# Kernel tuning notes

Measured on AMD Instinct MI355X. Metric: run time of the kernel, lower is better.

The kernel has to match this reference:

```python
import jax, jax.numpy as jnp
import numpy as np

B, N, NODE_DIM, COND_DIM, EDGE_DIM = 16, 256, 512, 512, 128
E_TOT = 262144  # total edges, divisible by B
EPS = 1e-5


def weight_norm(v, g):
    # torch weight_norm dim=0: per-output-row normalization. v: [out, in], g: [out]
    return v * (g / jnp.sqrt(jnp.sum(v * v, axis=1)))[:, None]


def setup_inputs() -> dict:
    key = jax.random.key(0)
    ks = jax.random.split(key, 12)
    node_feats = jax.random.normal(ks[0], (B, N, NODE_DIM), dtype=jnp.float32)
    cond_feats = jax.random.normal(ks[1], (B, COND_DIM), dtype=jnp.float32)
    edge_indexes = jnp.sort(jax.random.randint(ks[2], (E_TOT,), 0, B * N * N, dtype=jnp.int64))
    s_node = 1.0 / np.sqrt(NODE_DIM)
    s_cond = 1.0 / np.sqrt(COND_DIM)
    s_film = 1.0 / np.sqrt(2 * EDGE_DIM)
    return {
        "node_feats": node_feats,
        "cond_feats": cond_feats,
        "edge_indexes": edge_indexes,
        "v_node": jax.random.uniform(ks[3], (EDGE_DIM, NODE_DIM), jnp.float32, -s_node, s_node),
        "g_node": jnp.ones((EDGE_DIM,), jnp.float32),
        "b_node": jnp.zeros((EDGE_DIM,), jnp.float32),
        "v_cond": jax.random.uniform(ks[4], (2 * EDGE_DIM, COND_DIM), jnp.float32, -s_cond, s_cond),
        "g_cond": jnp.ones((2 * EDGE_DIM,), jnp.float32),
        "b_cond": jnp.zeros((2 * EDGE_DIM,), jnp.float32),
        "w_film": jax.random.uniform(ks[5], (EDGE_DIM, 2 * EDGE_DIM), jnp.float32, -s_film, s_film),
        "b_film": jnp.zeros((EDGE_DIM,), jnp.float32),
    }


def reference(node_feats, cond_feats, edge_indexes, v_node, g_node, b_node,
              v_cond, g_cond, b_cond, w_film, b_film):
    # node projection: Dropout(0) -> weight_norm Linear -> ReLU
    w_n = weight_norm(v_node, g_node)
    nodes = jax.nn.relu(jnp.einsum('bnd,ed->bne', node_feats, w_n) + b_node)  # [B,N,E]

    # cond projection -> gamma, beta
    w_c = weight_norm(v_cond, g_cond)
    gb = cond_feats @ w_c.T + b_cond  # [B, 2E]
    gamma = gb[:, :EDGE_DIM] + 1.0
    beta = gb[:, EDGE_DIM:]

    # gather edge endpoints directly (equivalent to materializing [B,N,N,2E] 'cat' then indexing)
    b_idx = edge_indexes // (N * N)
    i_idx = (edge_indexes // N) % N
    j_idx = edge_indexes % N
    fused = jnp.concatenate([nodes[b_idx, i_idx], nodes[b_idx, j_idx]], axis=-1)  # [E_TOT, 2E]

    # film_l: linear -> LayerNorm(no affine) -> FiLM -> ReLU, on view (B, E_TOT//B, E)
    x = fused @ w_film.T + b_film  # [E_TOT, EDGE_DIM]
    x = x.reshape(B, E_TOT // B, EDGE_DIM)
    mu = jnp.mean(x, axis=-1, keepdims=True)
    var = jnp.mean(jnp.square(x - mu), axis=-1, keepdims=True)
    x = (x - mu) * jax.lax.rsqrt(var + EPS)
    x = x * gamma[:, None, :] + beta[:, None, :]
    x = jax.nn.relu(x)
    return x.reshape(E_TOT, EDGE_DIM)
```

## Files before the change

### kernel.cpp

```cpp
#include <hip/hip_runtime.h>
#include <hip/hip_bf16.h>

typedef __bf16 bf16_t;
typedef bf16_t bf16x8 __attribute__((ext_vector_type(8)));
typedef float f32x4 __attribute__((ext_vector_type(4)));

#define NODE_DIM 512
#define COND_DIM 512
#define EDGE_DIM 128

__global__ __launch_bounds__(256) void cond_scales_kernel(
    const float* __restrict__ cond_feats, const float* __restrict__ v_cond,
    const float* __restrict__ g_cond, const float* __restrict__ b_cond,
    const float* __restrict__ v_node, const float* __restrict__ g_node,
    float* __restrict__ gamma, float* __restrict__ beta,
    float* __restrict__ scale_node)
{
    int lane = threadIdx.x & 63;
    int wv = threadIdx.x >> 6;
    int bid = blockIdx.x;
    if (bid < 1024) {
        int id = bid * 4 + wv;
        int b = id >> 8, n = id & 255;
        const float* cf = cond_feats + b * COND_DIM + lane * 8;
        const float* vc = v_cond + (size_t)n * COND_DIM + lane * 8;
        float dot = 0.f, sq = 0.f;
#pragma unroll
        for (int i = 0; i < 2; i++) {
            float4 c4 = ((const float4*)cf)[i];
            float4 v4 = ((const float4*)vc)[i];
            dot += c4.x * v4.x + c4.y * v4.y + c4.z * v4.z + c4.w * v4.w;
            sq  += v4.x * v4.x + v4.y * v4.y + v4.z * v4.z + v4.w * v4.w;
        }
#pragma unroll
        for (int o = 32; o > 0; o >>= 1) {
            dot += __shfl_xor(dot, o);
            sq  += __shfl_xor(sq, o);
        }
        if (lane == 0) {
            float val = dot * (g_cond[n] * rsqrtf(sq)) + b_cond[n];
            if (n < 128) gamma[b * 128 + n] = val + 1.0f;
            else         beta[b * 128 + (n - 128)] = val;
        }
    } else {
        int id = (bid - 1024) * 4 + wv;
        const float* vn = v_node + (size_t)id * NODE_DIM + lane * 8;
        float sq = 0.f;
#pragma unroll
        for (int i = 0; i < 2; i++) {
            float4 v4 = ((const float4*)vn)[i];
            sq += v4.x * v4.x + v4.y * v4.y + v4.z * v4.z + v4.w * v4.w;
        }
#pragma unroll
        for (int o = 32; o > 0; o >>= 1) sq += __shfl_xor(sq, o);
        if (lane == 0) scale_node[id] = g_node[id] * rsqrtf(sq);
    }
}

__global__ __launch_bounds__(256) void fused_gemm_kernel(
    const float* __restrict__ node_feats, const float* __restrict__ v_node,
    const float* __restrict__ b_node, const float* __restrict__ w_film,
    const float* __restrict__ scale_node, float* __restrict__ P)
{
    __shared__ __attribute__((aligned(16))) bf16_t A_s[64 * 40];
    __shared__ __attribute__((aligned(16))) bf16_t W_s[256 * 40];
    __shared__ __attribute__((aligned(16))) bf16_t N_s[64 * 136];

    int t = threadIdx.x;
    int lane = t & 63, wv = t >> 6;
    int m0 = blockIdx.x * 64;

    f32x4 zero4 = {0.f, 0.f, 0.f, 0.f};
    f32x4 acc[8];
#pragma unroll
    for (int i = 0; i < 8; i++) acc[i] = zero4;

    const int ar = t >> 2, ak = (t & 3) * 8;
    const int wn = t >> 1, wk = (t & 1) * 16;

    const int arow = wv * 16 + (lane & 15);
    const int kb = (lane >> 4) * 8;
    const int cl = lane & 15;

    for (int ks = 0; ks < 16; ks++) {
        int k0 = ks * 32;
        {
            const float* g = node_feats + (size_t)(m0 + ar) * NODE_DIM + k0 + ak;
            float4 x0 = ((const float4*)g)[0];
            float4 x1 = ((const float4*)g)[1];
            bf16x8 v;
            v[0] = (bf16_t)x0.x; v[1] = (bf16_t)x0.y; v[2] = (bf16_t)x0.z; v[3] = (bf16_t)x0.w;
            v[4] = (bf16_t)x1.x; v[5] = (bf16_t)x1.y; v[6] = (bf16_t)x1.z; v[7] = (bf16_t)x1.w;
            *(bf16x8*)&A_s[ar * 40 + ak] = v;
        }
        {
            const float* g = v_node + (size_t)wn * NODE_DIM + k0 + wk;
#pragma unroll
            for (int h = 0; h < 2; h++) {
                float4 x0 = ((const float4*)g)[2 * h];
                float4 x1 = ((const float4*)g)[2 * h + 1];
                bf16x8 v;
                v[0] = (bf16_t)x0.x; v[1] = (bf16_t)x0.y; v[2] = (bf16_t)x0.z; v[3] = (bf16_t)x0.w;
                v[4] = (bf16_t)x1.x; v[5] = (bf16_t)x1.y; v[6] = (bf16_t)x1.z; v[7] = (bf16_t)x1.w;
                *(bf16x8*)&W_s[wn * 40 + wk + h * 8] = v;
            }
        }
        __syncthreads();
        bf16x8 af = *(const bf16x8*)&A_s[arow * 40 + kb];
#pragma unroll
        for (int nt = 0; nt < 8; nt++) {
            bf16x8 bfr = *(const bf16x8*)&W_s[(nt * 16 + cl) * 40 + kb];
            acc[nt] = __builtin_amdgcn_mfma_f32_16x16x32_bf16(af, bfr, acc[nt], 0, 0, 0);
        }
        __syncthreads();
    }

    {
        int rbase = wv * 16 + ((lane >> 4) << 2);
#pragma unroll
        for (int nt = 0; nt < 8; nt++) {
            int col = nt * 16 + cl;
            float s = scale_node[col], bb = b_node[col];
#pragma unroll
            for (int r = 0; r < 4; r++) {
                float v = fmaxf(acc[nt][r] * s + bb, 0.f);
                N_s[(rbase + r) * 136 + col] = (bf16_t)v;
            }
        }
    }

    f32x4 acc2[16];
#pragma unroll
    for (int i = 0; i < 16; i++) acc2[i] = zero4;

    for (int ks = 0; ks < 4; ks++) {
        int k0 = ks * 32;
        __syncthreads();
        {
            const float* g = (t < 128) ? (w_film + (size_t)t * 256 + k0)
                                       : (w_film + (size_t)(t - 128) * 256 + 128 + k0);
#pragma unroll
            for (int h = 0; h < 4; h++) {
                float4 x0 = ((const float4*)g)[2 * h];
                float4 x1 = ((const float4*)g)[2 * h + 1];
                bf16x8 v;
                v[0] = (bf16_t)x0.x; v[1] = (bf16_t)x0.y; v[2] = (bf16_t)x0.z; v[3] = (bf16_t)x0.w;
                v[4] = (bf16_t)x1.x; v[5] = (bf16_t)x1.y; v[6] = (bf16_t)x1.z; v[7] = (bf16_t)x1.w;
                *(bf16x8*)&W_s[t * 40 + h * 8] = v;
            }
        }
        __syncthreads();
        bf16x8 af = *(const bf16x8*)&N_s[arow * 136 + k0 + kb];
#pragma unroll
        for (int nt = 0; nt < 16; nt++) {
            bf16x8 bfr = *(const bf16x8*)&W_s[(nt * 16 + cl) * 40 + kb];
            acc2[nt] = __builtin_amdgcn_mfma_f32_16x16x32_bf16(af, bfr, acc2[nt], 0, 0, 0);
        }
    }

    {
        int rbase = m0 + wv * 16 + ((lane >> 4) << 2);
#pragma unroll
        for (int nt = 0; nt < 16; nt++) {
            int col = nt * 16 + cl;
#pragma unroll
            for (int r = 0; r < 4; r++) {
                P[(size_t)(rbase + r) * 256 + col] = acc2[nt][r];
            }
        }
    }
}

__global__ __launch_bounds__(256) void edge_kernel(
    const int* __restrict__ edges, const float* __restrict__ P,
    const float* __restrict__ gamma, const float* __restrict__ beta,
    const float* __restrict__ b_film, float* __restrict__ out)
{
    int lane = threadIdx.x & 63;
    int wv = threadIdx.x >> 6;
    int r = blockIdx.x * 4 + wv;
    int e = edges[r];
    int ri = e >> 8;
    int rj = ((e >> 16) << 8) | (e & 255);
    int c = lane * 2;

    float2 p1 = *(const float2*)&P[(size_t)ri * 256 + c];
    float2 p2 = *(const float2*)&P[(size_t)rj * 256 + 128 + c];
    float2 bf = *(const float2*)&b_film[c];
    float tx = p1.x + p2.x + bf.x;
    float ty = p1.y + p2.y + bf.y;

    float s = tx + ty;
    float ss = tx * tx + ty * ty;
#pragma unroll
    for (int o = 32; o > 0; o >>= 1) {
        s  += __shfl_xor(s, o);
        ss += __shfl_xor(ss, o);
    }
    float mu = s * (1.0f / 128.0f);
    float var = ss * (1.0f / 128.0f) - mu * mu;
    float rs = rsqrtf(var + 1e-5f);

    int bb = r >> 14;
    float2 g  = *(const float2*)&gamma[bb * 128 + c];
    float2 be = *(const float2*)&beta[bb * 128 + c];
    float ox = fmaxf((tx - mu) * rs * g.x + be.x, 0.f);
    float oy = fmaxf((ty - mu) * rs * g.y + be.y, 0.f);
    *(float2*)&out[(size_t)r * 128 + c] = make_float2(ox, oy);
}

extern "C" void kernel_launch(void* const* d_in, const int* in_sizes, int n_in,
                              void* d_out, int out_size, void* d_ws, size_t ws_size,
                              hipStream_t stream) {
    const float* node_feats = (const float*)d_in[0];
    const float* cond_feats = (const float*)d_in[1];
    const int*   edges      = (const int*)d_in[2];
    const float* v_node     = (const float*)d_in[3];
    const float* g_node     = (const float*)d_in[4];
    const float* b_node     = (const float*)d_in[5];
    const float* v_cond     = (const float*)d_in[6];
    const float* g_cond     = (const float*)d_in[7];
    const float* b_cond     = (const float*)d_in[8];
    const float* w_film     = (const float*)d_in[9];
    const float* b_film     = (const float*)d_in[10];
    float* out = (float*)d_out;

    char* ws = (char*)d_ws;
    float* scale_node = (float*)(ws);
    float* gamma      = (float*)(ws + 4096);
    float* beta       = (float*)(ws + 4096 + 8192);
    float* P          = (float*)(ws + 32768);

    cond_scales_kernel<<<1056, 256, 0, stream>>>(cond_feats, v_cond, g_cond, b_cond,
                                                 v_node, g_node, gamma, beta, scale_node);
    fused_gemm_kernel<<<64, 256, 0, stream>>>(node_feats, v_node, b_node, w_film,
                                              scale_node, P);
    edge_kernel<<<65536, 256, 0, stream>>>(edges, P, gamma, beta, b_film, out);
}
```

Baseline: 232.9 us.

## Store projected node table in bf16 and process two edges per wavefront

The per-node projection table P is now written in bf16 instead of fp32, which halves the bytes gathered per edge. The edge kernel gives each half-wavefront one edge, using 4 columns per lane with float4 stores, and launches half as many blocks. Block indices are also permuted so that consecutive blocks cover strided row ranges. The cost is extra rounding error on P before the LayerNorm, and a different pattern of access locality.

```diff
diff --git a/kernel.cpp b/kernel.cpp
--- a/kernel.cpp
+++ b/kernel.cpp
@@ -3,6 +3,7 @@
 
 typedef __bf16 bf16_t;
 typedef bf16_t bf16x8 __attribute__((ext_vector_type(8)));
+typedef bf16_t bf16x4 __attribute__((ext_vector_type(4)));
 typedef float f32x4 __attribute__((ext_vector_type(4)));
 
 #define NODE_DIM 512
@@ -60,7 +61,7 @@
 __global__ __launch_bounds__(256) void fused_gemm_kernel(
     const float* __restrict__ node_feats, const float* __restrict__ v_node,
     const float* __restrict__ b_node, const float* __restrict__ w_film,
-    const float* __restrict__ scale_node, float* __restrict__ P)
+    const float* __restrict__ scale_node, bf16_t* __restrict__ P)
 {
     __shared__ __attribute__((aligned(16))) bf16_t A_s[64 * 40];
     __shared__ __attribute__((aligned(16))) bf16_t W_s[256 * 40];
@@ -165,48 +166,58 @@
             int col = nt * 16 + cl;
 #pragma unroll
             for (int r = 0; r < 4; r++) {
-                P[(size_t)(rbase + r) * 256 + col] = acc2[nt][r];
+                P[(size_t)(rbase + r) * 256 + col] = (bf16_t)acc2[nt][r];
             }
         }
     }
 }
 
 __global__ __launch_bounds__(256) void edge_kernel(
-    const int* __restrict__ edges, const float* __restrict__ P,
+    const int* __restrict__ edges, const bf16_t* __restrict__ P,
     const float* __restrict__ gamma, const float* __restrict__ beta,
     const float* __restrict__ b_film, float* __restrict__ out)
 {
-    int lane = threadIdx.x & 63;
-    int wv = threadIdx.x >> 6;
-    int r = blockIdx.x * 4 + wv;
+    int t = threadIdx.x;
+    int lane = t & 63, wv = t >> 6;
+    int v = (blockIdx.x & 7) * 4096 + (blockIdx.x >> 3);
+    int r = v * 8 + wv * 2 + (lane >> 5);
+    int hl = lane & 31;
+    int c = hl * 4;
+
+    int bb = v >> 11;
+    float4 g4  = *(const float4*)&gamma[bb * 128 + c];
+    float4 be4 = *(const float4*)&beta[bb * 128 + c];
+    float4 bf4 = *(const float4*)&b_film[c];
+
     int e = edges[r];
     int ri = e >> 8;
     int rj = ((e >> 16) << 8) | (e & 255);
-    int c = lane * 2;
-
-    float2 p1 = *(const float2*)&P[(size_t)ri * 256 + c];
-    float2 p2 = *(const float2*)&P[(size_t)rj * 256 + 128 + c];
-    float2 bf = *(const float2*)&b_film[c];
-    float tx = p1.x + p2.x + bf.x;
-    float ty = p1.y + p2.y + bf.y;
-
-    float s = tx + ty;
-    float ss = tx * tx + ty * ty;
-#pragma unroll
-    for (int o = 32; o > 0; o >>= 1) {
+
+    bf16x4 p1 = *(const bf16x4*)&P[(size_t)ri * 256 + c];
+    bf16x4 p2 = *(const bf16x4*)&P[(size_t)rj * 256 + 128 + c];
+
+    float x0 = (float)p1[0] + (float)p2[0] + bf4.x;
+    float x1 = (float)p1[1] + (float)p2[1] + bf4.y;
+    float x2 = (float)p1[2] + (float)p2[2] + bf4.z;
+    float x3 = (float)p1[3] + (float)p2[3] + bf4.w;
+
+    float s  = x0 + x1 + x2 + x3;
+    float ss = x0 * x0 + x1 * x1 + x2 * x2 + x3 * x3;
+#pragma unroll
+    for (int o = 16; o > 0; o >>= 1) {
         s  += __shfl_xor(s, o);
         ss += __shfl_xor(ss, o);
     }
-    float mu = s * (1.0f / 128.0f);
+    float mu  = s * (1.0f / 128.0f);
     float var = ss * (1.0f / 128.0f) - mu * mu;
-    float rs = rsqrtf(var + 1e-5f);
-
-    int bb = r >> 14;
-    float2 g  = *(const float2*)&gamma[bb * 128 + c];
-    float2 be = *(const float2*)&beta[bb * 128 + c];
-    float ox = fmaxf((tx - mu) * rs * g.x + be.x, 0.f);
-    float oy = fmaxf((ty - mu) * rs * g.y + be.y, 0.f);
-    *(float2*)&out[(size_t)r * 128 + c] = make_float2(ox, oy);
+    float rs  = rsqrtf(var + 1e-5f);
+
+    float4 o4;
+    o4.x = fmaxf((x0 - mu) * rs * g4.x + be4.x, 0.f);
+    o4.y = fmaxf((x1 - mu) * rs * g4.y + be4.y, 0.f);
+    o4.z = fmaxf((x2 - mu) * rs * g4.z + be4.z, 0.f);
+    o4.w = fmaxf((x3 - mu) * rs * g4.w + be4.w, 0.f);
+    *(float4*)&out[(size_t)r * 128 + c] = o4;
 }
 
 extern "C" void kernel_launch(void* const* d_in, const int* in_sizes, int n_in,
@@ -226,14 +237,14 @@
     float* out = (float*)d_out;
 
     char* ws = (char*)d_ws;
-    float* scale_node = (float*)(ws);
-    float* gamma      = (float*)(ws + 4096);
-    float* beta       = (float*)(ws + 4096 + 8192);
-    float* P          = (float*)(ws + 32768);
+    float*  scale_node = (float*)(ws);
+    float*  gamma      = (float*)(ws + 4096);
+    float*  beta       = (float*)(ws + 4096 + 8192);
+    bf16_t* P          = (bf16_t*)(ws + 32768);
 
     cond_scales_kernel<<<1056, 256, 0, stream>>>(cond_feats, v_cond, g_cond, b_cond,
                                                  v_node, g_node, gamma, beta, scale_node);
     fused_gemm_kernel<<<64, 256, 0, stream>>>(node_feats, v_node, b_node, w_film,
                                               scale_node, P);
-    edge_kernel<<<65536, 256, 0, stream>>>(edges, P, gamma, beta, b_film, out);
-}
+    edge_kernel<<<32768, 256, 0, stream>>>(edges, P, gamma, beta, b_film, out);
+}
```

Result: faster. 211.5 us (-9.2%).
